# Performance work log

Measured on AMD Instinct MI355X. Metric: run time of the kernel, lower is better.

The kernel has to match this reference:

```python
import jax, jax.numpy as jnp
import numpy as np

H = 32  # hidden_size

def _lstm_cell(x, h, c, Wih, Whh, bih, bhh):
    # PyTorch LSTMCell: gates order i, f, g, o
    g = x @ Wih.T + bih + h @ Whh.T + bhh  # [B, 4H]
    i, f, gg, o = jnp.split(g, 4, axis=-1)
    i = jax.nn.sigmoid(i); f = jax.nn.sigmoid(f)
    gg = jnp.tanh(gg);     o = jax.nn.sigmoid(o)
    c_new = f * c + i * gg
    h_new = o * jnp.tanh(c_new)
    return h_new, c_new


def setup_inputs() -> dict:
    key = jax.random.key(0)
    ks = jax.random.split(key, 16)
    B, T, I = 16384, 32, 27
    s_ih0 = 1.0 / np.sqrt(H)
    inp = {
        "obscured_tensor": jax.random.uniform(ks[0], (B, T, I), dtype=jnp.float32),
        "guessed_tensor": jax.random.uniform(ks[1], (B, 26), dtype=jnp.float32),
        # init_state uses xavier_normal on [B,H]: std = sqrt(2/(B+H))
        "h0": jax.random.normal(ks[2], (B, H), dtype=jnp.float32) * np.sqrt(2.0 / (B + H)),
        "c0": jax.random.normal(ks[3], (B, H), dtype=jnp.float32) * np.sqrt(2.0 / (B + H)),
        # layer 0 LSTMCell params (uniform(-1/sqrt(H), 1/sqrt(H)) like torch)
        "Wih0": jax.random.uniform(ks[4], (4 * H, I), jnp.float32, -s_ih0, s_ih0),
        "Whh0": jax.random.uniform(ks[5], (4 * H, H), jnp.float32, -s_ih0, s_ih0),
        "bih0": jax.random.uniform(ks[6], (4 * H,), jnp.float32, -s_ih0, s_ih0),
        "bhh0": jax.random.uniform(ks[7], (4 * H,), jnp.float32, -s_ih0, s_ih0),
        # layer 1 LSTMCell params
        "Wih1": jax.random.uniform(ks[8], (4 * H, H), jnp.float32, -s_ih0, s_ih0),
        "Whh1": jax.random.uniform(ks[9], (4 * H, H), jnp.float32, -s_ih0, s_ih0),
        "bih1": jax.random.uniform(ks[10], (4 * H,), jnp.float32, -s_ih0, s_ih0),
        "bhh1": jax.random.uniform(ks[11], (4 * H,), jnp.float32, -s_ih0, s_ih0),
        # fc: Linear(H + 26, 26)
        "Wfc": jax.random.uniform(ks[12], (26, H + 26), jnp.float32, -1.0 / np.sqrt(H + 26), 1.0 / np.sqrt(H + 26)),
        "bfc": jax.random.uniform(ks[13], (26,), jnp.float32, -1.0 / np.sqrt(H + 26), 1.0 / np.sqrt(H + 26)),
    }
    return inp


def reference(obscured_tensor, guessed_tensor, h0, c0,
              Wih0, Whh0, bih0, bhh0, Wih1, Whh1, bih1, bhh1, Wfc, bfc):
    B, T, _ = obscured_tensor.shape
    # faithful to torch: .view(T, B, -1) is a raw reshape, not a transpose
    xs = obscured_tensor.reshape(T, B, -1)  # [T, B, 27]

    def step(carry, x):
        h1, c1, h2, c2, hsum = carry
        h1, c1 = _lstm_cell(x, h1, c1, Wih0, Whh0, bih0, bhh0)
        h2, c2 = _lstm_cell(h1, h2, c2, Wih1, Whh1, bih1, bhh1)
        return (h1, c1, h2, c2, hsum + h2), None

    # init_state aliases the same xavier-initialized tensor for all layers
    init = (h0, c0, h0, c0, jnp.zeros_like(h0))
    (h1, c1, h2, c2, hsum), _ = jax.lax.scan(step, init, xs)

    # 'avg' aggregation: mean over time of concat(h_top, guessed);
    # guessed is time-constant so mean(concat) == concat(mean(h), guessed)
    agg = jnp.concatenate([hsum / T, guessed_tensor], axis=1)  # [B, H+26]
    logits = agg @ Wfc.T + bfc
    return logits, jax.nn.sigmoid(logits)
```

## Files before the change

kernel.cpp:

```cpp
#include <hip/hip_runtime.h>
#include <hip/hip_bf16.h>

#define NB 16384
#define NT 32
#define NI 27
#define NH 32
#define NG 26

typedef __attribute__((ext_vector_type(8))) short bf16x8;
typedef __attribute__((ext_vector_type(4))) float f32x4;
typedef __attribute__((ext_vector_type(4))) int   i32x4;

#define MFMA(a, b, c) __builtin_amdgcn_mfma_f32_16x16x32_bf16((a), (b), (c), 0, 0, 0)
#define SWZ_XOR8 0x201F

static __device__ __forceinline__ int pack2(float lo, float hi) {
    unsigned short a = __builtin_bit_cast(unsigned short, __float2bfloat16(lo));
    unsigned short b = __builtin_bit_cast(unsigned short, __float2bfloat16(hi));
    return (int)(((unsigned)b << 16) | (unsigned)a);
}

static __device__ __forceinline__ i32x4 make_wfrag(const float* __restrict__ W,
                                                   int rowlen, int nrows, int row,
                                                   int g4, int kbase, bool perm) {
    int w[4];
#pragma unroll
    for (int q = 0; q < 4; ++q) {
        int klo = perm ? (16 * (q >> 1) + 4 * g4 + ((2 * q) & 3))
                       : (kbase + 8 * g4 + 2 * q);
        int khi = klo + 1;
        float lo = (row < nrows && klo < rowlen) ? W[row * rowlen + klo] : 0.0f;
        float hi = (row < nrows && khi < rowlen) ? W[row * rowlen + khi] : 0.0f;
        w[q] = pack2(lo, hi);
    }
    i32x4 v = { w[0], w[1], w[2], w[3] };
    return v;
}

static __device__ __forceinline__ i32x4 make_wfrag_xb(const float* __restrict__ W,
                                                      const float* __restrict__ bi,
                                                      const float* __restrict__ bh,
                                                      int row, int g4) {
    int w[4];
#pragma unroll
    for (int q = 0; q < 4; ++q) {
        int klo = 8 * g4 + 2 * q;
        int khi = klo + 1;
        float lo = (klo < NI) ? W[row * NI + klo] : ((klo == NI) ? bi[row] + bh[row] : 0.0f);
        float hi = (khi < NI) ? W[row * NI + khi] : ((khi == NI) ? bi[row] + bh[row] : 0.0f);
        w[q] = pack2(lo, hi);
    }
    i32x4 v = { w[0], w[1], w[2], w[3] };
    return v;
}

static __device__ __forceinline__ bf16x8 join_bfrag(const float hn[4], bool mh1) {
    int p0 = pack2(hn[0], hn[1]);
    int p1 = pack2(hn[2], hn[3]);
    int q0 = __builtin_amdgcn_ds_swizzle(p0, SWZ_XOR8);
    int q1 = __builtin_amdgcn_ds_swizzle(p1, SWZ_XOR8);
    i32x4 v = { mh1 ? q0 : p0, mh1 ? q1 : p1, mh1 ? p0 : q0, mh1 ? p1 : q1 };
    return __builtin_bit_cast(bf16x8, v);
}

__global__ __launch_bounds__(256, 2)
void lstm_lds(const float* __restrict__ X,
              const float* __restrict__ Gu,
              const float* __restrict__ H0, const float* __restrict__ C0,
              const float* __restrict__ Wih0, const float* __restrict__ Whh0,
              const float* __restrict__ bih0, const float* __restrict__ bhh0,
              const float* __restrict__ Wih1, const float* __restrict__ Whh1,
              const float* __restrict__ bih1, const float* __restrict__ bhh1,
              const float* __restrict__ Wfc, const float* __restrict__ bfc,
              float* __restrict__ out)
{
    __shared__ i32x4 sA0x[512], sA0h[512], sA1i[512], sA1h[512];
    __shared__ f32x4 sB1[32];
    __shared__ i32x4 sAfc[256];

    const int tid  = threadIdx.x;
    const int lane = tid & 63;
    const int bl   = lane & 15;
    const int g4   = lane >> 4;
    const int k0   = 8 * g4;
    const int wid  = blockIdx.x * 4 + (tid >> 6);
    const int batch = wid * 8 + (bl & 7);
    const bool mh1 = (bl >> 3) != 0;

#pragma unroll 1
    for (int slot = tid; slot < 512; slot += 256) {
        int m = slot >> 6, ln = slot & 63;
        int bs = ln & 15, gs = ln >> 4;
        sA0x[slot] = make_wfrag_xb(Wih0, bih0, bhh0, 16 * m + bs, gs);
        sA0h[slot] = make_wfrag(Whh0, NH, 4 * NH, 16 * m + bs, gs, 0, true);
        sA1i[slot] = make_wfrag(Wih1, NH, 4 * NH, 16 * m + bs, gs, 0, true);
        sA1h[slot] = make_wfrag(Whh1, NH, 4 * NH, 16 * m + bs, gs, 0, true);
    }
    if (tid < 32) {
        int m = tid >> 2, q4 = tid & 3;
        f32x4 b;
#pragma unroll
        for (int r = 0; r < 4; ++r) {
            int gr = 16 * m + 4 * q4 + r;
            b[r] = bih1[gr] + bhh1[gr];
        }
        sB1[tid] = b;
    }
    {
        int part = tid >> 7, m2 = (tid >> 6) & 1, ln = tid & 63;
        int bs = ln & 15, gs = ln >> 4;
        sAfc[tid] = part ? make_wfrag(Wfc, NH + NG, NG, 16 * m2 + bs, gs, NH, false)
                         : make_wfrag(Wfc, NH + NG, NG, 16 * m2 + bs, gs, 0, true);
    }
    __syncthreads();

    const float* h0p = H0 + (size_t)batch * NH;
    const float* c0p = C0 + (size_t)batch * NH;
    i32x4 hv = { pack2(h0p[4 * g4],          h0p[4 * g4 + 1]),
                 pack2(h0p[4 * g4 + 2],      h0p[4 * g4 + 3]),
                 pack2(h0p[16 + 4 * g4],     h0p[16 + 4 * g4 + 1]),
                 pack2(h0p[16 + 4 * g4 + 2], h0p[16 + 4 * g4 + 3]) };
    bf16x8 h1f = __builtin_bit_cast(bf16x8, hv);
    bf16x8 h2f = h1f;
    float c1[4], c2[4], hsum[4];
#pragma unroll
    for (int r = 0; r < 4; ++r) {
        float c = c0p[(mh1 ? 16 : 0) + 4 * g4 + r];
        c1[r] = c; c2[r] = c; hsum[r] = 0.0f;
    }

    float xn[8];
    {
        const float* xp = X + (size_t)batch * NI;
#pragma unroll
        for (int j = 0; j < 8; ++j) {
            int k = k0 + j;
            xn[j] = (k < NI) ? xp[k] : ((k == NI) ? 1.0f : 0.0f);
        }
    }

    const f32x4 zero4 = { 0.0f, 0.0f, 0.0f, 0.0f };

#pragma unroll 1
    for (int t = 0; t < NT; ++t) {
        int xw[4];
#pragma unroll
        for (int q = 0; q < 4; ++q) xw[q] = pack2(xn[2 * q], xn[2 * q + 1]);
        i32x4 xv = { xw[0], xw[1], xw[2], xw[3] };
        bf16x8 xf = __builtin_bit_cast(bf16x8, xv);
        if (t + 1 < NT) {
            const float* xp = X + ((size_t)(t + 1) * NB + batch) * NI;
#pragma unroll
            for (int j = 0; j < 8; ++j) {
                int k = k0 + j;
                xn[j] = (k < NI) ? xp[k] : ((k == NI) ? 1.0f : 0.0f);
            }
        }

        f32x4 g[8];
#pragma unroll
        for (int m = 0; m < 8; ++m)
            g[m] = MFMA(__builtin_bit_cast(bf16x8, sA0x[m * 64 + lane]), xf, zero4);
#pragma unroll
        for (int m = 0; m < 8; ++m)
            g[m] = MFMA(__builtin_bit_cast(bf16x8, sA0h[m * 64 + lane]), h1f, g[m]);
        float hn1[4];
#pragma unroll
        for (int r = 0; r < 4; ++r) {
            float gi_ = mh1 ? g[1][r] : g[0][r];
            float gf_ = mh1 ? g[3][r] : g[2][r];
            float gg_ = mh1 ? g[5][r] : g[4][r];
            float go_ = mh1 ? g[7][r] : g[6][r];
            float ei = __expf(-gi_);
            float ef = __expf(-gf_);
            float eg = __expf(-2.0f * gg_);
            float eo = __expf(-go_);
            float ig = (1.0f - eg) * __builtin_amdgcn_rcpf(fmaf(ei, eg, ei) + eg + 1.0f);
            float fv = __builtin_amdgcn_rcpf(1.0f + ef);
            float c  = fmaf(fv, c1[r], ig);
            c1[r] = c;
            float ec = __expf(-2.0f * c);
            hn1[r] = (1.0f - ec) * __builtin_amdgcn_rcpf(fmaf(eo, ec, eo) + ec + 1.0f);
        }
        h1f = join_bfrag(hn1, mh1);

#pragma unroll
        for (int m = 0; m < 8; ++m)
            g[m] = MFMA(__builtin_bit_cast(bf16x8, sA1i[m * 64 + lane]), h1f, sB1[m * 4 + g4]);
#pragma unroll
        for (int m = 0; m < 8; ++m)
            g[m] = MFMA(__builtin_bit_cast(bf16x8, sA1h[m * 64 + lane]), h2f, g[m]);
        float hn2[4];
#pragma unroll
        for (int r = 0; r < 4; ++r) {
            float gi_ = mh1 ? g[1][r] : g[0][r];
            float gf_ = mh1 ? g[3][r] : g[2][r];
            float gg_ = mh1 ? g[5][r] : g[4][r];
            float go_ = mh1 ? g[7][r] : g[6][r];
            float ei = __expf(-gi_);
            float ef = __expf(-gf_);
            float eg = __expf(-2.0f * gg_);
            float eo = __expf(-go_);
            float ig = (1.0f - eg) * __builtin_amdgcn_rcpf(fmaf(ei, eg, ei) + eg + 1.0f);
            float fv = __builtin_amdgcn_rcpf(1.0f + ef);
            float c  = fmaf(fv, c2[r], ig);
            c2[r] = c;
            float ec = __expf(-2.0f * c);
            float h  = (1.0f - ec) * __builtin_amdgcn_rcpf(fmaf(eo, ec, eo) + ec + 1.0f);
            hn2[r] = h;
            hsum[r] += h;
        }
        h2f = join_bfrag(hn2, mh1);
    }

    float hs[4];
#pragma unroll
    for (int r = 0; r < 4; ++r) hs[r] = hsum[r] * (1.0f / NT);
    bf16x8 hsf = join_bfrag(hs, mh1);

    int gw[4];
    {
        const float* gp = Gu + (size_t)batch * NG;
#pragma unroll
        for (int q = 0; q < 4; ++q) {
            int k = k0 + 2 * q;
            float lo = (k     < NG) ? gp[k]     : 0.0f;
            float hi = (k + 1 < NG) ? gp[k + 1] : 0.0f;
            gw[q] = pack2(lo, hi);
        }
    }
    i32x4 gv_ = { gw[0], gw[1], gw[2], gw[3] };
    bf16x8 guf = __builtin_bit_cast(bf16x8, gv_);

    f32x4 L[2];
#pragma unroll
    for (int m2 = 0; m2 < 2; ++m2)
        L[m2] = MFMA(__builtin_bit_cast(bf16x8, sAfc[m2 * 64 + lane]), hsf, zero4);
#pragma unroll
    for (int m2 = 0; m2 < 2; ++m2)
        L[m2] = MFMA(__builtin_bit_cast(bf16x8, sAfc[128 + m2 * 64 + lane]), guf, L[m2]);

    if (bl < 8) {
#pragma unroll
        for (int m2 = 0; m2 < 2; ++m2)
#pragma unroll
            for (int r = 0; r < 4; ++r) {
                int row = 16 * m2 + 4 * g4 + r;
                if (row < NG) {
                    float v = L[m2][r] + bfc[row];
                    out[(size_t)batch * NG + row] = v;
                    out[(size_t)NB * NG + (size_t)batch * NG + row] =
                        __builtin_amdgcn_rcpf(1.0f + __expf(-v));
                }
            }
    }
}

extern "C" void kernel_launch(void* const* d_in, const int* in_sizes, int n_in,
                              void* d_out, int out_size, void* d_ws, size_t ws_size,
                              hipStream_t stream) {
    const float* X    = (const float*)d_in[0];
    const float* Gu   = (const float*)d_in[1];
    const float* H0   = (const float*)d_in[2];
    const float* C0   = (const float*)d_in[3];
    const float* Wih0 = (const float*)d_in[4];
    const float* Whh0 = (const float*)d_in[5];
    const float* bih0 = (const float*)d_in[6];
    const float* bhh0 = (const float*)d_in[7];
    const float* Wih1 = (const float*)d_in[8];
    const float* Whh1 = (const float*)d_in[9];
    const float* bih1 = (const float*)d_in[10];
    const float* bhh1 = (const float*)d_in[11];
    const float* Wfc  = (const float*)d_in[12];
    const float* bfc  = (const float*)d_in[13];
    float* out = (float*)d_out;

    dim3 grid(NB / 8 / 4), block(256);
    hipLaunchKernelGGL(lstm_lds, grid, block, 0, stream,
                       X, Gu, H0, C0, Wih0, Whh0, bih0, bhh0,
                       Wih1, Whh1, bih1, bhh1, Wfc, bfc, out);
}
```

Baseline: 67.95 us.

## Process two batch groups per wave to reuse weight fragments and add ILP

Each wavefront now handles 16 batch rows as two independent 8-row groups. Each LDS weight fragment is loaded once and fed to two MFMAs, and the two recurrences interleave to hide latency. The grid is halved, and the launch bounds no longer request 2 blocks per CU. The cost is higher register pressure and fewer resident waves, so latency hiding depends on in-wave ILP.

After: 81.48 us. 19.9% more time.

```diff
diff --git a/kernel.cpp b/kernel.cpp
--- a/kernel.cpp
+++ b/kernel.cpp
@@ -63,16 +63,37 @@
     return __builtin_bit_cast(bf16x8, v);
 }
 
-__global__ __launch_bounds__(256, 2)
-void lstm_lds(const float* __restrict__ X,
-              const float* __restrict__ Gu,
-              const float* __restrict__ H0, const float* __restrict__ C0,
-              const float* __restrict__ Wih0, const float* __restrict__ Whh0,
-              const float* __restrict__ bih0, const float* __restrict__ bhh0,
-              const float* __restrict__ Wih1, const float* __restrict__ Whh1,
-              const float* __restrict__ bih1, const float* __restrict__ bhh1,
-              const float* __restrict__ Wfc, const float* __restrict__ bfc,
-              float* __restrict__ out)
+static __device__ __forceinline__ void act4(const f32x4 g[8], float cst[4], float hn[4],
+                                            bool mh1) {
+#pragma unroll
+    for (int r = 0; r < 4; ++r) {
+        float gi_ = mh1 ? g[1][r] : g[0][r];
+        float gf_ = mh1 ? g[3][r] : g[2][r];
+        float gg_ = mh1 ? g[5][r] : g[4][r];
+        float go_ = mh1 ? g[7][r] : g[6][r];
+        float ei = __expf(-gi_);
+        float ef = __expf(-gf_);
+        float eg = __expf(-2.0f * gg_);
+        float eo = __expf(-go_);
+        float ig = (1.0f - eg) * __builtin_amdgcn_rcpf(fmaf(ei, eg, ei) + eg + 1.0f);
+        float fv = __builtin_amdgcn_rcpf(1.0f + ef);
+        float c  = fmaf(fv, cst[r], ig);
+        cst[r] = c;
+        float ec = __expf(-2.0f * c);
+        hn[r] = (1.0f - ec) * __builtin_amdgcn_rcpf(fmaf(eo, ec, eo) + ec + 1.0f);
+    }
+}
+
+__global__ __launch_bounds__(256)
+void lstm_dual(const float* __restrict__ X,
+               const float* __restrict__ Gu,
+               const float* __restrict__ H0, const float* __restrict__ C0,
+               const float* __restrict__ Wih0, const float* __restrict__ Whh0,
+               const float* __restrict__ bih0, const float* __restrict__ bhh0,
+               const float* __restrict__ Wih1, const float* __restrict__ Whh1,
+               const float* __restrict__ bih1, const float* __restrict__ bhh1,
+               const float* __restrict__ Wfc, const float* __restrict__ bfc,
+               float* __restrict__ out)
 {
     __shared__ i32x4 sA0x[512], sA0h[512], sA1i[512], sA1h[512];
     __shared__ f32x4 sB1[32];
@@ -84,7 +105,8 @@
     const int g4   = lane >> 4;
     const int k0   = 8 * g4;
     const int wid  = blockIdx.x * 4 + (tid >> 6);
-    const int batch = wid * 8 + (bl & 7);
+    const int batchA = wid * 16 + (bl & 7);
+    const int batchB = batchA + 8;
     const bool mh1 = (bl >> 3) != 0;
 
 #pragma unroll 1
@@ -97,11 +119,11 @@
         sA1h[slot] = make_wfrag(Whh1, NH, 4 * NH, 16 * m + bs, gs, 0, true);
     }
     if (tid < 32) {
-        int m = tid >> 2, q4 = tid & 3;
+        int m = tid >> 2, q4_ = tid & 3;
         f32x4 b;
 #pragma unroll
         for (int r = 0; r < 4; ++r) {
-            int gr = 16 * m + 4 * q4 + r;
+            int gr = 16 * m + 4 * q4_ + r;
             b[r] = bih1[gr] + bhh1[gr];
         }
         sB1[tid] = b;
@@ -114,28 +136,35 @@
     }
     __syncthreads();
 
-    const float* h0p = H0 + (size_t)batch * NH;
-    const float* c0p = C0 + (size_t)batch * NH;
-    i32x4 hv = { pack2(h0p[4 * g4],          h0p[4 * g4 + 1]),
-                 pack2(h0p[4 * g4 + 2],      h0p[4 * g4 + 3]),
-                 pack2(h0p[16 + 4 * g4],     h0p[16 + 4 * g4 + 1]),
-                 pack2(h0p[16 + 4 * g4 + 2], h0p[16 + 4 * g4 + 3]) };
-    bf16x8 h1f = __builtin_bit_cast(bf16x8, hv);
-    bf16x8 h2f = h1f;
-    float c1[4], c2[4], hsum[4];
+    const float* hA = H0 + (size_t)batchA * NH;
+    const float* hB = H0 + (size_t)batchB * NH;
+    const float* cA = C0 + (size_t)batchA * NH;
+    const float* cB = C0 + (size_t)batchB * NH;
+    i32x4 hvA = { pack2(hA[4 * g4], hA[4 * g4 + 1]), pack2(hA[4 * g4 + 2], hA[4 * g4 + 3]),
+                  pack2(hA[16 + 4 * g4], hA[16 + 4 * g4 + 1]),
+                  pack2(hA[16 + 4 * g4 + 2], hA[16 + 4 * g4 + 3]) };
+    i32x4 hvB = { pack2(hB[4 * g4], hB[4 * g4 + 1]), pack2(hB[4 * g4 + 2], hB[4 * g4 + 3]),
+                  pack2(hB[16 + 4 * g4], hB[16 + 4 * g4 + 1]),
+                  pack2(hB[16 + 4 * g4 + 2], hB[16 + 4 * g4 + 3]) };
+    bf16x8 h1fA = __builtin_bit_cast(bf16x8, hvA), h2fA = h1fA;
+    bf16x8 h1fB = __builtin_bit_cast(bf16x8, hvB), h2fB = h1fB;
+    float c1A[4], c2A[4], hsA[4], c1B[4], c2B[4], hsB[4];
 #pragma unroll
     for (int r = 0; r < 4; ++r) {
-        float c = c0p[(mh1 ? 16 : 0) + 4 * g4 + r];
-        c1[r] = c; c2[r] = c; hsum[r] = 0.0f;
-    }
-
-    float xn[8];
+        int u = (mh1 ? 16 : 0) + 4 * g4 + r;
+        c1A[r] = cA[u]; c2A[r] = c1A[r]; hsA[r] = 0.0f;
+        c1B[r] = cB[u]; c2B[r] = c1B[r]; hsB[r] = 0.0f;
+    }
+
+    float xnA[8], xnB[8];
     {
-        const float* xp = X + (size_t)batch * NI;
+        const float* xa = X + (size_t)batchA * NI;
+        const float* xb = X + (size_t)batchB * NI;
 #pragma unroll
         for (int j = 0; j < 8; ++j) {
             int k = k0 + j;
-            xn[j] = (k < NI) ? xp[k] : ((k == NI) ? 1.0f : 0.0f);
+            xnA[j] = (k < NI) ? xa[k] : ((k == NI) ? 1.0f : 0.0f);
+            xnB[j] = (k < NI) ? xb[k] : ((k == NI) ? 1.0f : 0.0f);
         }
     }
 
@@ -143,102 +172,105 @@
 
 #pragma unroll 1
     for (int t = 0; t < NT; ++t) {
-        int xw[4];
-#pragma unroll
-        for (int q = 0; q < 4; ++q) xw[q] = pack2(xn[2 * q], xn[2 * q + 1]);
-        i32x4 xv = { xw[0], xw[1], xw[2], xw[3] };
-        bf16x8 xf = __builtin_bit_cast(bf16x8, xv);
+        int xwA[4], xwB[4];
+#pragma unroll
+        for (int q = 0; q < 4; ++q) {
+            xwA[q] = pack2(xnA[2 * q], xnA[2 * q + 1]);
+            xwB[q] = pack2(xnB[2 * q], xnB[2 * q + 1]);
+        }
+        i32x4 xvA = { xwA[0], xwA[1], xwA[2], xwA[3] };
+        i32x4 xvB = { xwB[0], xwB[1], xwB[2], xwB[3] };
+        bf16x8 xfA = __builtin_bit_cast(bf16x8, xvA);
+        bf16x8 xfB = __builtin_bit_cast(bf16x8, xvB);
         if (t + 1 < NT) {
-            const float* xp = X + ((size_t)(t + 1) * NB + batch) * NI;
+            const float* xa = X + ((size_t)(t + 1) * NB + batchA) * NI;
+            const float* xb = X + ((size_t)(t + 1) * NB + batchB) * NI;
 #pragma unroll
             for (int j = 0; j < 8; ++j) {
                 int k = k0 + j;
-                xn[j] = (k < NI) ? xp[k] : ((k == NI) ? 1.0f : 0.0f);
+                xnA[j] = (k < NI) ? xa[k] : ((k == NI) ? 1.0f : 0.0f);
+                xnB[j] = (k < NI) ? xb[k] : ((k == NI) ? 1.0f : 0.0f);
             }
         }
 
-        f32x4 g[8];
-#pragma unroll
-        for (int m = 0; m < 8; ++m)
-            g[m] = MFMA(__builtin_bit_cast(bf16x8, sA0x[m * 64 + lane]), xf, zero4);
-#pragma unroll
-        for (int m = 0; m < 8; ++m)
-            g[m] = MFMA(__builtin_bit_cast(bf16x8, sA0h[m * 64 + lane]), h1f, g[m]);
-        float hn1[4];
-#pragma unroll
-        for (int r = 0; r < 4; ++r) {
-            float gi_ = mh1 ? g[1][r] : g[0][r];
-            float gf_ = mh1 ? g[3][r] : g[2][r];
-            float gg_ = mh1 ? g[5][r] : g[4][r];
-            float go_ = mh1 ? g[7][r] : g[6][r];
-            float ei = __expf(-gi_);
-            float ef = __expf(-gf_);
-            float eg = __expf(-2.0f * gg_);
-            float eo = __expf(-go_);
-            float ig = (1.0f - eg) * __builtin_amdgcn_rcpf(fmaf(ei, eg, ei) + eg + 1.0f);
-            float fv = __builtin_amdgcn_rcpf(1.0f + ef);
-            float c  = fmaf(fv, c1[r], ig);
-            c1[r] = c;
-            float ec = __expf(-2.0f * c);
-            hn1[r] = (1.0f - ec) * __builtin_amdgcn_rcpf(fmaf(eo, ec, eo) + ec + 1.0f);
-        }
-        h1f = join_bfrag(hn1, mh1);
-
-#pragma unroll
-        for (int m = 0; m < 8; ++m)
-            g[m] = MFMA(__builtin_bit_cast(bf16x8, sA1i[m * 64 + lane]), h1f, sB1[m * 4 + g4]);
-#pragma unroll
-        for (int m = 0; m < 8; ++m)
-            g[m] = MFMA(__builtin_bit_cast(bf16x8, sA1h[m * 64 + lane]), h2f, g[m]);
-        float hn2[4];
-#pragma unroll
-        for (int r = 0; r < 4; ++r) {
-            float gi_ = mh1 ? g[1][r] : g[0][r];
-            float gf_ = mh1 ? g[3][r] : g[2][r];
-            float gg_ = mh1 ? g[5][r] : g[4][r];
-            float go_ = mh1 ? g[7][r] : g[6][r];
-            float ei = __expf(-gi_);
-            float ef = __expf(-gf_);
-            float eg = __expf(-2.0f * gg_);
-            float eo = __expf(-go_);
-            float ig = (1.0f - eg) * __builtin_amdgcn_rcpf(fmaf(ei, eg, ei) + eg + 1.0f);
-            float fv = __builtin_amdgcn_rcpf(1.0f + ef);
-            float c  = fmaf(fv, c2[r], ig);
-            c2[r] = c;
-            float ec = __expf(-2.0f * c);
-            float h  = (1.0f - ec) * __builtin_amdgcn_rcpf(fmaf(eo, ec, eo) + ec + 1.0f);
-            hn2[r] = h;
-            hsum[r] += h;
-        }
-        h2f = join_bfrag(hn2, mh1);
-    }
-
-    float hs[4];
-#pragma unroll
-    for (int r = 0; r < 4; ++r) hs[r] = hsum[r] * (1.0f / NT);
-    bf16x8 hsf = join_bfrag(hs, mh1);
-
-    int gw[4];
+        f32x4 gA[8], gB[8];
+#pragma unroll
+        for (int m = 0; m < 8; ++m) {
+            bf16x8 w = __builtin_bit_cast(bf16x8, sA0x[m * 64 + lane]);
+            gA[m] = MFMA(w, xfA, zero4);
+            gB[m] = MFMA(w, xfB, zero4);
+        }
+#pragma unroll
+        for (int m = 0; m < 8; ++m) {
+            bf16x8 w = __builtin_bit_cast(bf16x8, sA0h[m * 64 + lane]);
+            gA[m] = MFMA(w, h1fA, gA[m]);
+            gB[m] = MFMA(w, h1fB, gB[m]);
+        }
+        float hn1A[4], hn1B[4];
+        act4(gA, c1A, hn1A, mh1);
+        act4(gB, c1B, hn1B, mh1);
+        h1fA = join_bfrag(hn1A, mh1);
+        h1fB = join_bfrag(hn1B, mh1);
+
+#pragma unroll
+        for (int m = 0; m < 8; ++m) {
+            bf16x8 w = __builtin_bit_cast(bf16x8, sA1i[m * 64 + lane]);
+            f32x4 b = sB1[m * 4 + g4];
+            gA[m] = MFMA(w, h1fA, b);
+            gB[m] = MFMA(w, h1fB, b);
+        }
+#pragma unroll
+        for (int m = 0; m < 8; ++m) {
+            bf16x8 w = __builtin_bit_cast(bf16x8, sA1h[m * 64 + lane]);
+            gA[m] = MFMA(w, h2fA, gA[m]);
+            gB[m] = MFMA(w, h2fB, gB[m]);
+        }
+        float hn2A[4], hn2B[4];
+        act4(gA, c2A, hn2A, mh1);
+        act4(gB, c2B, hn2B, mh1);
+#pragma unroll
+        for (int r = 0; r < 4; ++r) { hsA[r] += hn2A[r]; hsB[r] += hn2B[r]; }
+        h2fA = join_bfrag(hn2A, mh1);
+        h2fB = join_bfrag(hn2B, mh1);
+    }
+
+    float hA4[4], hB4[4];
+#pragma unroll
+    for (int r = 0; r < 4; ++r) { hA4[r] = hsA[r] * (1.0f / NT); hB4[r] = hsB[r] * (1.0f / NT); }
+    bf16x8 hsfA = join_bfrag(hA4, mh1);
+    bf16x8 hsfB = join_bfrag(hB4, mh1);
+
+    int gwA[4], gwB[4];
     {
-        const float* gp = Gu + (size_t)batch * NG;
+        const float* ga = Gu + (size_t)batchA * NG;
+        const float* gb = Gu + (size_t)batchB * NG;
 #pragma unroll
         for (int q = 0; q < 4; ++q) {
             int k = k0 + 2 * q;
-            float lo = (k     < NG) ? gp[k]     : 0.0f;
-            float hi = (k + 1 < NG) ? gp[k + 1] : 0.0f;
-            gw[q] = pack2(lo, hi);
-        }
-    }
-    i32x4 gv_ = { gw[0], gw[1], gw[2], gw[3] };
-    bf16x8 guf = __builtin_bit_cast(bf16x8, gv_);
-
-    f32x4 L[2];
-#pragma unroll
-    for (int m2 = 0; m2 < 2; ++m2)
-        L[m2] = MFMA(__builtin_bit_cast(bf16x8, sAfc[m2 * 64 + lane]), hsf, zero4);
-#pragma unroll
-    for (int m2 = 0; m2 < 2; ++m2)
-        L[m2] = MFMA(__builtin_bit_cast(bf16x8, sAfc[128 + m2 * 64 + lane]), guf, L[m2]);
+            float loA = (k < NG) ? ga[k] : 0.0f, hiA = (k + 1 < NG) ? ga[k + 1] : 0.0f;
+            float loB = (k < NG) ? gb[k] : 0.0f, hiB = (k + 1 < NG) ? gb[k + 1] : 0.0f;
+            gwA[q] = pack2(loA, hiA);
+            gwB[q] = pack2(loB, hiB);
+        }
+    }
+    i32x4 gvA = { gwA[0], gwA[1], gwA[2], gwA[3] };
+    i32x4 gvB = { gwB[0], gwB[1], gwB[2], gwB[3] };
+    bf16x8 gufA = __builtin_bit_cast(bf16x8, gvA);
+    bf16x8 gufB = __builtin_bit_cast(bf16x8, gvB);
+
+    f32x4 LA[2], LB[2];
+#pragma unroll
+    for (int m2 = 0; m2 < 2; ++m2) {
+        bf16x8 w = __builtin_bit_cast(bf16x8, sAfc[m2 * 64 + lane]);
+        LA[m2] = MFMA(w, hsfA, zero4);
+        LB[m2] = MFMA(w, hsfB, zero4);
+    }
+#pragma unroll
+    for (int m2 = 0; m2 < 2; ++m2) {
+        bf16x8 w = __builtin_bit_cast(bf16x8, sAfc[128 + m2 * 64 + lane]);
+        LA[m2] = MFMA(w, gufA, LA[m2]);
+        LB[m2] = MFMA(w, gufB, LB[m2]);
+    }
 
     if (bl < 8) {
 #pragma unroll
@@ -247,10 +279,14 @@
             for (int r = 0; r < 4; ++r) {
                 int row = 16 * m2 + 4 * g4 + r;
                 if (row < NG) {
-                    float v = L[m2][r] + bfc[row];
-                    out[(size_t)batch * NG + row] = v;
-                    out[(size_t)NB * NG + (size_t)batch * NG + row] =
-                        __builtin_amdgcn_rcpf(1.0f + __expf(-v));
+                    float vA = LA[m2][r] + bfc[row];
+                    float vB = LB[m2][r] + bfc[row];
+                    out[(size_t)batchA * NG + row] = vA;
+                    out[(size_t)batchB * NG + row] = vB;
+                    out[(size_t)NB * NG + (size_t)batchA * NG + row] =
+                        __builtin_amdgcn_rcpf(1.0f + __expf(-vA));
+                    out[(size_t)NB * NG + (size_t)batchB * NG + row] =
+                        __builtin_amdgcn_rcpf(1.0f + __expf(-vB));
                 }
             }
     }
@@ -275,8 +311,8 @@
     const float* bfc  = (const float*)d_in[13];
     float* out = (float*)d_out;
 
-    dim3 grid(NB / 8 / 4), block(256);
-    hipLaunchKernelGGL(lstm_lds, grid, block, 0, stream,
+    dim3 grid(NB / 16 / 4), block(256);
+    hipLaunchKernelGGL(lstm_dual, grid, block, 0, stream,
                        X, Gu, H0, C0, Wih0, Whh0, bih0, bhh0,
                        Wih1, Whh1, bih1, bhh1, Wfc, bfc, out);
 }
```

## Fold log2e scaling into weights, merge gate reciprocals, prepack x to bf16

Applied to the files above, without the earlier changes.

The log2(e) factor (twice that for the g gate) is folded into the weight and bias fragments at load time, so the activations can call the native exp2 instruction directly and skip a multiply per exponential. The cell-state update combines the input and forget sigmoids into one reciprocal of P*Q instead of two. The prefetched x values are packed to bf16 as soon as they load, which lowers register use, and the launch-bounds minimum-occupancy hint is removed. The extra scaling before bf16 rounding changes the rounding slightly, and the product P*Q could overflow for large gate magnitudes.

Result: slower. 80.15 us (+18.0%).

```diff
diff --git a/kernel.cpp b/kernel.cpp
--- a/kernel.cpp
+++ b/kernel.cpp
@@ -7,12 +7,23 @@
 #define NH 32
 #define NG 26
 
+#define L2E  1.4426950408889634f
+#define NL2E2 -2.885390081777927f
+
 typedef __attribute__((ext_vector_type(8))) short bf16x8;
 typedef __attribute__((ext_vector_type(4))) float f32x4;
 typedef __attribute__((ext_vector_type(4))) int   i32x4;
 
 #define MFMA(a, b, c) __builtin_amdgcn_mfma_f32_16x16x32_bf16((a), (b), (c), 0, 0, 0)
 #define SWZ_XOR8 0x201F
+
+static __device__ __forceinline__ float exp2x(float x) {
+#if __has_builtin(__builtin_amdgcn_exp2f)
+    return __builtin_amdgcn_exp2f(x);
+#else
+    return __expf(x * 0.6931471805599453f);
+#endif
+}
 
 static __device__ __forceinline__ int pack2(float lo, float hi) {
     unsigned short a = __builtin_bit_cast(unsigned short, __float2bfloat16(lo));
@@ -20,17 +31,21 @@
     return (int)(((unsigned)b << 16) | (unsigned)a);
 }
 
+static __device__ __forceinline__ float rowscale(int row) {
+    return (((row >> 5) & 3) == 2) ? 2.0f * L2E : L2E;
+}
+
 static __device__ __forceinline__ i32x4 make_wfrag(const float* __restrict__ W,
                                                    int rowlen, int nrows, int row,
-                                                   int g4, int kbase, bool perm) {
+                                                   int g4, int kbase, bool perm, float s) {
     int w[4];
 #pragma unroll
     for (int q = 0; q < 4; ++q) {
         int klo = perm ? (16 * (q >> 1) + 4 * g4 + ((2 * q) & 3))
                        : (kbase + 8 * g4 + 2 * q);
         int khi = klo + 1;
-        float lo = (row < nrows && klo < rowlen) ? W[row * rowlen + klo] : 0.0f;
-        float hi = (row < nrows && khi < rowlen) ? W[row * rowlen + khi] : 0.0f;
+        float lo = (row < nrows && klo < rowlen) ? W[row * rowlen + klo] * s : 0.0f;
+        float hi = (row < nrows && khi < rowlen) ? W[row * rowlen + khi] * s : 0.0f;
         w[q] = pack2(lo, hi);
     }
     i32x4 v = { w[0], w[1], w[2], w[3] };
@@ -40,14 +55,16 @@
 static __device__ __forceinline__ i32x4 make_wfrag_xb(const float* __restrict__ W,
                                                       const float* __restrict__ bi,
                                                       const float* __restrict__ bh,
-                                                      int row, int g4) {
+                                                      int row, int g4, float s) {
     int w[4];
 #pragma unroll
     for (int q = 0; q < 4; ++q) {
         int klo = 8 * g4 + 2 * q;
         int khi = klo + 1;
-        float lo = (klo < NI) ? W[row * NI + klo] : ((klo == NI) ? bi[row] + bh[row] : 0.0f);
-        float hi = (khi < NI) ? W[row * NI + khi] : ((khi == NI) ? bi[row] + bh[row] : 0.0f);
+        float lo = (klo < NI) ? W[row * NI + klo] * s
+                              : ((klo == NI) ? (bi[row] + bh[row]) * s : 0.0f);
+        float hi = (khi < NI) ? W[row * NI + khi] * s
+                              : ((khi == NI) ? (bi[row] + bh[row]) * s : 0.0f);
         w[q] = pack2(lo, hi);
     }
     i32x4 v = { w[0], w[1], w[2], w[3] };
@@ -63,16 +80,38 @@
     return __builtin_bit_cast(bf16x8, v);
 }
 
-__global__ __launch_bounds__(256, 2)
-void lstm_lds(const float* __restrict__ X,
-              const float* __restrict__ Gu,
-              const float* __restrict__ H0, const float* __restrict__ C0,
-              const float* __restrict__ Wih0, const float* __restrict__ Whh0,
-              const float* __restrict__ bih0, const float* __restrict__ bhh0,
-              const float* __restrict__ Wih1, const float* __restrict__ Whh1,
-              const float* __restrict__ bih1, const float* __restrict__ bhh1,
-              const float* __restrict__ Wfc, const float* __restrict__ bfc,
-              float* __restrict__ out)
+static __device__ __forceinline__ void act4(const f32x4 g[8], float cst[4], float hn[4],
+                                            bool mh1) {
+#pragma unroll
+    for (int r = 0; r < 4; ++r) {
+        float gi_ = mh1 ? g[1][r] : g[0][r];
+        float gf_ = mh1 ? g[3][r] : g[2][r];
+        float gg_ = mh1 ? g[5][r] : g[4][r];
+        float go_ = mh1 ? g[7][r] : g[6][r];
+        float ei = exp2x(-gi_);
+        float ef = exp2x(-gf_);
+        float eg = exp2x(-gg_);
+        float eo = exp2x(-go_);
+        float P  = fmaf(ei, eg, ei) + eg + 1.0f;
+        float Q  = 1.0f + ef;
+        float c  = fmaf(cst[r], P, (1.0f - eg) * Q) * __builtin_amdgcn_rcpf(P * Q);
+        cst[r] = c;
+        float ec = exp2x(c * NL2E2);
+        float R  = fmaf(eo, ec, eo) + ec + 1.0f;
+        hn[r] = (1.0f - ec) * __builtin_amdgcn_rcpf(R);
+    }
+}
+
+__global__ __launch_bounds__(256)
+void lstm_x2(const float* __restrict__ X,
+             const float* __restrict__ Gu,
+             const float* __restrict__ H0, const float* __restrict__ C0,
+             const float* __restrict__ Wih0, const float* __restrict__ Whh0,
+             const float* __restrict__ bih0, const float* __restrict__ bhh0,
+             const float* __restrict__ Wih1, const float* __restrict__ Whh1,
+             const float* __restrict__ bih1, const float* __restrict__ bhh1,
+             const float* __restrict__ Wfc, const float* __restrict__ bfc,
+             float* __restrict__ out)
 {
     __shared__ i32x4 sA0x[512], sA0h[512], sA1i[512], sA1h[512];
     __shared__ f32x4 sB1[32];
@@ -91,26 +130,28 @@
     for (int slot = tid; slot < 512; slot += 256) {
         int m = slot >> 6, ln = slot & 63;
         int bs = ln & 15, gs = ln >> 4;
-        sA0x[slot] = make_wfrag_xb(Wih0, bih0, bhh0, 16 * m + bs, gs);
-        sA0h[slot] = make_wfrag(Whh0, NH, 4 * NH, 16 * m + bs, gs, 0, true);
-        sA1i[slot] = make_wfrag(Wih1, NH, 4 * NH, 16 * m + bs, gs, 0, true);
-        sA1h[slot] = make_wfrag(Whh1, NH, 4 * NH, 16 * m + bs, gs, 0, true);
+        int row = 16 * m + bs;
+        float s = rowscale(row);
+        sA0x[slot] = make_wfrag_xb(Wih0, bih0, bhh0, row, gs, s);
+        sA0h[slot] = make_wfrag(Whh0, NH, 4 * NH, row, gs, 0, true, s);
+        sA1i[slot] = make_wfrag(Wih1, NH, 4 * NH, row, gs, 0, true, s);
+        sA1h[slot] = make_wfrag(Whh1, NH, 4 * NH, row, gs, 0, true, s);
     }
     if (tid < 32) {
-        int m = tid >> 2, q4 = tid & 3;
+        int m = tid >> 2, q4_ = tid & 3;
         f32x4 b;
 #pragma unroll
         for (int r = 0; r < 4; ++r) {
-            int gr = 16 * m + 4 * q4 + r;
-            b[r] = bih1[gr] + bhh1[gr];
+            int gr = 16 * m + 4 * q4_ + r;
+            b[r] = (bih1[gr] + bhh1[gr]) * rowscale(gr);
         }
         sB1[tid] = b;
     }
     {
         int part = tid >> 7, m2 = (tid >> 6) & 1, ln = tid & 63;
         int bs = ln & 15, gs = ln >> 4;
-        sAfc[tid] = part ? make_wfrag(Wfc, NH + NG, NG, 16 * m2 + bs, gs, NH, false)
-                         : make_wfrag(Wfc, NH + NG, NG, 16 * m2 + bs, gs, 0, true);
+        sAfc[tid] = part ? make_wfrag(Wfc, NH + NG, NG, 16 * m2 + bs, gs, NH, false, 1.0f)
+                         : make_wfrag(Wfc, NH + NG, NG, 16 * m2 + bs, gs, 0, true, 1.0f);
     }
     __syncthreads();
 
@@ -129,13 +170,15 @@
         c1[r] = c; c2[r] = c; hsum[r] = 0.0f;
     }
 
-    float xn[8];
+    int xn[4];
     {
         const float* xp = X + (size_t)batch * NI;
 #pragma unroll
-        for (int j = 0; j < 8; ++j) {
-            int k = k0 + j;
-            xn[j] = (k < NI) ? xp[k] : ((k == NI) ? 1.0f : 0.0f);
+        for (int q = 0; q < 4; ++q) {
+            int klo = k0 + 2 * q, khi = klo + 1;
+            float lo = (klo < NI) ? xp[klo] : ((klo == NI) ? 1.0f : 0.0f);
+            float hi = (khi < NI) ? xp[khi] : ((khi == NI) ? 1.0f : 0.0f);
+            xn[q] = pack2(lo, hi);
         }
     }
 
@@ -143,17 +186,16 @@
 
 #pragma unroll 1
     for (int t = 0; t < NT; ++t) {
-        int xw[4];
-#pragma unroll
-        for (int q = 0; q < 4; ++q) xw[q] = pack2(xn[2 * q], xn[2 * q + 1]);
-        i32x4 xv = { xw[0], xw[1], xw[2], xw[3] };
+        i32x4 xv = { xn[0], xn[1], xn[2], xn[3] };
         bf16x8 xf = __builtin_bit_cast(bf16x8, xv);
         if (t + 1 < NT) {
             const float* xp = X + ((size_t)(t + 1) * NB + batch) * NI;
 #pragma unroll
-            for (int j = 0; j < 8; ++j) {
-                int k = k0 + j;
-                xn[j] = (k < NI) ? xp[k] : ((k == NI) ? 1.0f : 0.0f);
+            for (int q = 0; q < 4; ++q) {
+                int klo = k0 + 2 * q, khi = klo + 1;
+                float lo = (klo < NI) ? xp[klo] : ((klo == NI) ? 1.0f : 0.0f);
+                float hi = (khi < NI) ? xp[khi] : ((khi == NI) ? 1.0f : 0.0f);
+                xn[q] = pack2(lo, hi);
             }
         }
 
@@ -165,23 +207,7 @@
         for (int m = 0; m < 8; ++m)
             g[m] = MFMA(__builtin_bit_cast(bf16x8, sA0h[m * 64 + lane]), h1f, g[m]);
         float hn1[4];
-#pragma unroll
-        for (int r = 0; r < 4; ++r) {
-            float gi_ = mh1 ? g[1][r] : g[0][r];
-            float gf_ = mh1 ? g[3][r] : g[2][r];
-            float gg_ = mh1 ? g[5][r] : g[4][r];
-            float go_ = mh1 ? g[7][r] : g[6][r];
-            float ei = __expf(-gi_);
-            float ef = __expf(-gf_);
-            float eg = __expf(-2.0f * gg_);
-            float eo = __expf(-go_);
-            float ig = (1.0f - eg) * __builtin_amdgcn_rcpf(fmaf(ei, eg, ei) + eg + 1.0f);
-            float fv = __builtin_amdgcn_rcpf(1.0f + ef);
-            float c  = fmaf(fv, c1[r], ig);
-            c1[r] = c;
-            float ec = __expf(-2.0f * c);
-            hn1[r] = (1.0f - ec) * __builtin_amdgcn_rcpf(fmaf(eo, ec, eo) + ec + 1.0f);
-        }
+        act4(g, c1, hn1, mh1);
         h1f = join_bfrag(hn1, mh1);
 
 #pragma unroll
@@ -191,25 +217,9 @@
         for (int m = 0; m < 8; ++m)
             g[m] = MFMA(__builtin_bit_cast(bf16x8, sA1h[m * 64 + lane]), h2f, g[m]);
         float hn2[4];
-#pragma unroll
-        for (int r = 0; r < 4; ++r) {
-            float gi_ = mh1 ? g[1][r] : g[0][r];
-            float gf_ = mh1 ? g[3][r] : g[2][r];
-            float gg_ = mh1 ? g[5][r] : g[4][r];
-            float go_ = mh1 ? g[7][r] : g[6][r];
-            float ei = __expf(-gi_);
-            float ef = __expf(-gf_);
-            float eg = __expf(-2.0f * gg_);
-            float eo = __expf(-go_);
-            float ig = (1.0f - eg) * __builtin_amdgcn_rcpf(fmaf(ei, eg, ei) + eg + 1.0f);
-            float fv = __builtin_amdgcn_rcpf(1.0f + ef);
-            float c  = fmaf(fv, c2[r], ig);
-            c2[r] = c;
-            float ec = __expf(-2.0f * c);
-            float h  = (1.0f - ec) * __builtin_amdgcn_rcpf(fmaf(eo, ec, eo) + ec + 1.0f);
-            hn2[r] = h;
-            hsum[r] += h;
-        }
+        act4(g, c2, hn2, mh1);
+#pragma unroll
+        for (int r = 0; r < 4; ++r) hsum[r] += hn2[r];
         h2f = join_bfrag(hn2, mh1);
     }
 
@@ -250,7 +260,7 @@
                     float v = L[m2][r] + bfc[row];
                     out[(size_t)batch * NG + row] = v;
                     out[(size_t)NB * NG + (size_t)batch * NG + row] =
-                        __builtin_amdgcn_rcpf(1.0f + __expf(-v));
+                        __builtin_amdgcn_rcpf(1.0f + exp2x(-v * L2E));
                 }
             }
     }
@@ -276,7 +286,7 @@
     float* out = (float*)d_out;
 
     dim3 grid(NB / 8 / 4), block(256);
-    hipLaunchKernelGGL(lstm_lds, grid, block, 0, stream,
+    hipLaunchKernelGGL(lstm_x2, grid, block, 0, stream,
                        X, Gu, H0, C0, Wih0, Whh0, bih0, bhh0,
                        Wih1, Whh1, bih1, bhh1, Wfc, bfc, out);
 }
```
